# Kernel tuning notes

Measured on AMD Instinct MI355X. Metric: run time of the kernel, lower is better.

## Reference

```python
import jax, jax.numpy as jnp
import numpy as np

GROUPS = 4
BN_EPS = 1e-5


def conv2d(x, w, pad=0):
    return jax.lax.conv_general_dilated(x, w, (1, 1), [(pad, pad), (pad, pad)],
                                        dimension_numbers=('NCHW', 'OIHW', 'NCHW'))


def bn_infer(x, g, b, m, v):
    s = g * jax.lax.rsqrt(v + BN_EPS)
    return x * s[None, :, None, None] + (b - m * s)[None, :, None, None]


def refine_residual(x, w1, w3a, g, b, m, v, w3b):
    # RefineResidual(has_relu=True): 1x1 -> ConvBnRelu(3x3) -> 3x3 conv, residual, relu
    x1 = conv2d(x, w1)
    t = jax.nn.relu(bn_infer(conv2d(x1, w3a, pad=1), g, b, m, v))
    t = conv2d(t, w3b, pad=1)
    return jax.nn.relu(t + x1)


def grid_edges(H, W):
    # 4-connected pixel grid: right + down neighbors
    idx = np.arange(H * W).reshape(H, W)
    eu = np.concatenate([idx[:, :-1].ravel(), idx[:-1, :].ravel()]).astype(np.int32)
    ev = np.concatenate([idx[:, 1:].ravel(), idx[1:, :].ravel()]).astype(np.int32)
    return jnp.asarray(eu), jnp.asarray(ev)


def boruvka_mst(w, eu, ev, N):
    # Boruvka MST over the grid graph; returns bool mask over edges (N-1 True).
    E = w.shape[0]
    nodes = jnp.arange(N, dtype=jnp.int32)
    order = jnp.argsort(w).astype(jnp.int32)                  # edge ids by weight (unique ranks)
    rank = jnp.zeros(E, jnp.int32).at[order].set(jnp.arange(E, dtype=jnp.int32))
    BIG = jnp.int32(E)
    R = int(np.ceil(np.log2(max(N, 2)))) + 2

    def flatten(p):
        return jax.lax.fori_loop(0, R, lambda _, q: q[q], p)

    def body(_, state):
        parent, mst = state
        cu, cv = parent[eu], parent[ev]
        key = jnp.where(cu != cv, rank, BIG)
        cmin = jnp.minimum(jax.ops.segment_min(key, cu, num_segments=N),
                           jax.ops.segment_min(key, cv, num_segments=N))
        valid = cmin < BIG
        e = order[jnp.minimum(cmin, E - 1)]                   # min outgoing edge per component
        mst = mst.at[e].max(valid)
        other = jnp.where(cu[e] == nodes, cv[e], cu[e])
        pnew = jnp.where(valid, other, nodes)
        # break mutual (2-cycle) merges: smaller label becomes root
        pnew = jnp.where((pnew[pnew] == nodes) & (nodes < pnew), nodes, pnew)
        return flatten(pnew), mst

    _, mst = jax.lax.fori_loop(0, R + 2, body, (nodes, jnp.zeros(E, bool)))
    return mst


def root_and_depth(mst, eu, ev, N):
    # BFS-root the tree at node 0 -> parent pointers, then depth by pointer doubling.
    pn = jnp.full(N, -1, jnp.int32).at[0].set(0)

    def bfs(_, pn):
        vis = pn >= 0
        a = mst & vis[eu] & (~vis[ev])
        b = mst & vis[ev] & (~vis[eu])
        pn = pn.at[ev].max(jnp.where(a, eu, jnp.int32(-1)))
        pn = pn.at[eu].max(jnp.where(b, ev, jnp.int32(-1)))
        return pn

    pn = jax.lax.fori_loop(0, N, bfs, pn)
    R = int(np.ceil(np.log2(max(N, 2)))) + 2
    d0 = (jnp.arange(N) != 0).astype(jnp.int32)

    def dbl(_, s):
        d, p = s
        return d + d[p], p[p]

    depth, _ = jax.lax.fori_loop(0, R, dbl, (d0, pn))
    return pn, depth


def tree_filter_group(x, w, pn, depth):
    # Exact O(N) two-pass tree filter: y_i = sum_j prod(path weights i->j) x_j.
    # x: [N, C] (ones channel appended by caller), w: [N] edge weight to parent.
    N = x.shape[0]
    notroot = jnp.arange(N) != 0

    def up(i, agg):                                           # leaves -> root
        lev = N - 1 - i
        sel = (depth == lev) & notroot
        return agg.at[pn].add(jnp.where(sel[:, None], w[:, None] * agg, 0.0))

    agg = jax.lax.fori_loop(0, N - 1, up, x)

    def down(lev, F):                                         # root -> leaves
        cand = agg + w[:, None] * (F[pn] - w[:, None] * agg)
        return jnp.where(((depth == lev) & notroot)[:, None], cand, F)

    return jax.lax.fori_loop(1, N, down, agg)


def tree_filter_2d(feat, emb, pn, depth):
    # Grouped normalized tree filtering (TreeFilter2D): per-group edge affinity
    # exp(-||e_v - e_parent(v)||^2); normalize by filtering an all-ones channel.
    B, C, H, W = feat.shape
    N = H * W
    f = feat.reshape(B, GROUPS, C // GROUPS, N)
    e = emb.reshape(B, GROUPS, -1, N)

    def per_batch(fb, eb, pnb, db):
        w = jnp.exp(-jnp.sum((eb - eb[:, :, pnb]) ** 2, axis=1))   # [G, N]
        x = jnp.concatenate([fb, jnp.ones_like(fb[:, :1])], axis=1)
        x = jnp.swapaxes(x, 1, 2)                                  # [G, N, Cg+1]
        out = jax.vmap(lambda xg, wg: tree_filter_group(xg, wg, pnb, db))(x, w)
        y = out[..., :-1] / out[..., -1:]
        return jnp.swapaxes(y, 1, 2)

    out = jax.vmap(per_batch)(f, e, pn, depth)
    return out.reshape(B, C, H, W)


def _forward(fm, last_fm, lat_w1, lat_w3a, lat_g, lat_b, lat_m, lat_v, lat_w3b,
             ref_w1, ref_w3a, ref_g, ref_b, ref_m, ref_v, ref_w3b, emb_w):
    B, Cb, H, W = fm.shape
    N = H * W
    eu, ev = grid_edges(H, W)
    latent = refine_residual(fm, lat_w1, lat_w3a, lat_g, lat_b, lat_m, lat_v, lat_w3b)
    # MinimumSpanningTree(norm2_distance) on backbone features fm
    f = fm.reshape(B, Cb, N)
    dist = jnp.sum((f[:, :, eu] - f[:, :, ev]) ** 2, axis=1)       # [B, E]
    mst = jax.vmap(lambda d: boruvka_mst(d, eu, ev, N))(dist)
    pn, depth = jax.vmap(lambda m: root_and_depth(m, eu, ev, N))(mst)
    embed = conv2d(last_fm, emb_w)                                 # embed_layer (1x1, no bn/relu)
    fusion = latent + tree_filter_2d(last_fm, embed, pn, depth)
    return refine_residual(fusion, ref_w1, ref_w3a, ref_g, ref_b, ref_m, ref_v, ref_w3b)


def setup_inputs() -> dict:
    key = jax.random.key(0)
    ks = jax.random.split(key, 12)
    B, Cb, Cbiz, Cemb, H, W = 2, 1024, 64, 32, 32, 32
    r = lambda k, s: jax.random.normal(k, s, jnp.float32) * 0.05
    return dict(
        fm=jax.random.normal(ks[0], (B, Cb, H, W), jnp.float32),
        last_fm=jax.random.normal(ks[1], (B, Cbiz, H, W), jnp.float32),
        lat_w1=r(ks[2], (Cbiz, Cb, 1, 1)),
        lat_w3a=r(ks[3], (Cbiz, Cbiz, 3, 3)),
        lat_g=jnp.ones(Cbiz, jnp.float32),
        lat_b=jnp.zeros(Cbiz, jnp.float32),
        lat_m=jnp.zeros(Cbiz, jnp.float32),
        lat_v=jax.random.uniform(ks[4], (Cbiz,), jnp.float32, 0.5, 1.5),
        lat_w3b=r(ks[5], (Cbiz, Cbiz, 3, 3)),
        ref_w1=r(ks[6], (Cbiz, Cbiz, 1, 1)),
        ref_w3a=r(ks[7], (Cbiz, Cbiz, 3, 3)),
        ref_g=jnp.ones(Cbiz, jnp.float32),
        ref_b=jnp.zeros(Cbiz, jnp.float32),
        ref_m=jnp.zeros(Cbiz, jnp.float32),
        ref_v=jax.random.uniform(ks[8], (Cbiz,), jnp.float32, 0.5, 1.5),
        ref_w3b=r(ks[9], (Cbiz, Cbiz, 3, 3)),
        emb_w=r(ks[10], (Cemb, Cbiz, 1, 1)),
    )


def reference(fm, last_fm, lat_w1, lat_w3a, lat_g, lat_b, lat_m, lat_v, lat_w3b,
              ref_w1, ref_w3a, ref_g, ref_b, ref_m, ref_v, ref_w3b, emb_w):
    return _forward(fm, last_fm, lat_w1, lat_w3a, lat_g, lat_b, lat_m, lat_v, lat_w3b,
                    ref_w1, ref_w3a, ref_g, ref_b, ref_m, ref_v, ref_w3b, emb_w)
```

## Files before the change

### kernel.cpp

```cpp
#include <hip/hip_runtime.h>
#include <hip/hip_bf16.h>

#define NN 1024
#define EE 1984

__device__ __forceinline__ void edge_uv(int e, int* u, int* v) {
    if (e < 992) {
        int r = e / 31, c = e - r * 31;
        *u = r * 32 + c; *v = *u + 1;
    } else {
        *u = e - 992; *v = *u + 32;
    }
}

__device__ void conv1x1_tile(const float* __restrict__ in, const float* __restrict__ in2,
                             const float* __restrict__ w,
                             float* __restrict__ out, int CIN, int Cout,
                             int b, int co0, int n0, float* red) {
    int tid = threadIdx.x;
    int px = tid & 63, kc = tid >> 6;
    int kcu = __builtin_amdgcn_readfirstlane(kc);
    int KCH = CIN >> 4;
    size_t ibase = (size_t)b * CIN * NN + n0 + px;
    const float* wr = w + (size_t)co0 * CIN;
    float acc[8] = {0.f,0.f,0.f,0.f,0.f,0.f,0.f,0.f};
    for (int ci = kcu * KCH; ci < kcu * KCH + KCH; ++ci) {
        float xv = in[ibase + (size_t)ci * NN];
        if (in2) xv += in2[ibase + (size_t)ci * NN];
#pragma unroll
        for (int j = 0; j < 8; ++j)
            acc[j] += wr[j * CIN + ci] * xv;
    }
#pragma unroll
    for (int j = 0; j < 8; ++j) red[j * 1024 + tid] = acc[j];
    __syncthreads();
    for (int s = 8; s >= 1; s >>= 1) {
        if (kc < s) {
#pragma unroll
            for (int j = 0; j < 8; ++j)
                red[j * 1024 + kc * 64 + px] += red[j * 1024 + (kc + s) * 64 + px];
        }
        __syncthreads();
    }
    if (kc == 0) {
        size_t ob = ((size_t)b * Cout + co0) * NN + n0 + px;
#pragma unroll
        for (int j = 0; j < 8; ++j) out[ob + (size_t)j * NN] = red[j * 1024 + px];
    }
}

__device__ void dist_tile(const float* __restrict__ fm, float* __restrict__ dist,
                          int b, int eb, float* red) {
    int tid = threadIdx.x;
    int le = tid & 63, kc = tid >> 6;
    int kcu = __builtin_amdgcn_readfirstlane(kc);
    int e = eb * 64 + le;
    int u, v; edge_uv(e, &u, &v);
    const float* fp = fm + (size_t)b * 1024 * NN;
    float s = 0.f;
    for (int c = kcu * 64; c < kcu * 64 + 64; ++c) {
        float d = fp[(size_t)c * NN + u] - fp[(size_t)c * NN + v];
        s += d * d;
    }
    red[tid] = s;
    __syncthreads();
    for (int ss = 8; ss >= 1; ss >>= 1) {
        if (kc < ss) red[kc * 64 + le] += red[(kc + ss) * 64 + le];
        __syncthreads();
    }
    if (kc == 0) dist[b * EE + e] = red[le];
}

__device__ void conv3x3_body(const float* __restrict__ in, const float* __restrict__ w,
                             const float* __restrict__ gg, const float* __restrict__ bb,
                             const float* __restrict__ mm, const float* __restrict__ vv,
                             const float* __restrict__ res, float* __restrict__ out,
                             int mode, int b, int co, int r0, float* pl) {
    int tid = threadIdx.x;
    const float* ip = in + (size_t)b * 64 * NN;
    const float* wp = w + (size_t)co * 64 * 9;
    int r = tid >> 5, c = tid & 31;
    float acc = 0.f;
    for (int h = 0; h < 2; ++h) {
        __syncthreads();
        for (int i4 = tid; i4 < 32 * 80; i4 += 256) {
            int ci = i4 / 80, o = i4 - ci * 80;
            int row = r0 - 1 + (o >> 3), c4 = (o & 7) << 2;
            float4 val = make_float4(0.f, 0.f, 0.f, 0.f);
            if (row >= 0 && row < 32)
                val = *(const float4*)&ip[(size_t)(h * 32 + ci) * NN + row * 32 + c4];
            *(float4*)&pl[ci * 320 + (o >> 3) * 32 + c4] = val;
        }
        __syncthreads();
        for (int ci = 0; ci < 32; ++ci) {
            float wv[9];
#pragma unroll
            for (int q = 0; q < 9; ++q) wv[q] = wp[(h * 32 + ci) * 9 + q];
            float s = 0.f;
#pragma unroll
            for (int dy = 0; dy < 3; ++dy) {
                const float* row = &pl[ci * 320 + (r + dy) * 32];
#pragma unroll
                for (int dx = -1; dx <= 1; ++dx) {
                    int cc = c + dx;
                    float xv = (cc >= 0 && cc < 32) ? row[cc] : 0.f;
                    s += wv[dy * 3 + (dx + 1)] * xv;
                }
            }
            acc += s;
        }
    }
    float val;
    size_t op = ((size_t)b * 64 + co) * NN + r0 * 32 + tid;
    if (mode == 0) {
        float sc = gg[co] * rsqrtf(vv[co] + 1e-5f);
        val = acc * sc + (bb[co] - mm[co] * sc);
    } else {
        val = acc + res[op];
    }
    out[op] = fmaxf(val, 0.f);
}

struct MstS {
    unsigned long long minkey[NN];
    unsigned long long ekey[EE];
    int parent[NN], pnw[NN], pn[NN], dep[NN], scr[NN], elist[NN];
    int mstm[EE];
    int cnt, cnt2;
};

__device__ void mst_body_1024(const float* __restrict__ dist, int b, MstS* S,
                              int* __restrict__ pn_g, int* __restrict__ maxd_g,
                              int* __restrict__ ord_g, int* __restrict__ off_g) {
    int tid = threadIdx.x;
    const float* wb = dist + b * EE;
    S->parent[tid] = tid;
    S->minkey[tid] = ~0ULL;
    for (int e = tid; e < EE; e += 1024) {
        S->mstm[e] = 0;
        S->ekey[e] = ((unsigned long long)__float_as_uint(wb[e]) << 32) | (unsigned)e;
    }
    if (tid == 0) { S->cnt = 0; S->cnt2 = 0; }
    __syncthreads();

    int r = tid >> 5, c = tid & 31;
    for (int round = 0; round < 14; ++round) {
        int pv = S->parent[tid];
        unsigned long long mk = ~0ULL;
        if (c < 31 && S->parent[tid + 1] != pv) {
            unsigned long long k = S->ekey[r * 31 + c];
            if (k < mk) mk = k;
        }
        if (c > 0 && S->parent[tid - 1] != pv) {
            unsigned long long k = S->ekey[r * 31 + c - 1];
            if (k < mk) mk = k;
        }
        if (r < 31 && S->parent[tid + 32] != pv) {
            unsigned long long k = S->ekey[992 + r * 32 + c];
            if (k < mk) mk = k;
        }
        if (r > 0 && S->parent[tid - 32] != pv) {
            unsigned long long k = S->ekey[992 + (r - 1) * 32 + c];
            if (k < mk) mk = k;
        }
        if (mk != ~0ULL) atomicMin(&S->minkey[pv], mk);
        __syncthreads();
        int np;
        unsigned long long sel = S->minkey[tid];
        S->minkey[tid] = ~0ULL;
        if (sel != ~0ULL) {
            int e = (int)(sel & 0xffffffffULL);
            if (atomicExch(&S->mstm[e], 1) == 0) atomicAdd(&S->cnt, 1);
            int eu, ev; edge_uv(e, &eu, &ev);
            int cu = S->parent[eu], cv = S->parent[ev];
            np = (cu == tid) ? cv : cu;
        } else np = tid;
        S->pnw[tid] = np;
        __syncthreads();
        int q = S->pnw[tid];
        int pq = S->pnw[q];
        S->parent[tid] = (pq == tid && tid < q) ? tid : q;
        for (;;) {
            int ch = 0;
            int p = S->parent[tid];
            int pp = S->parent[p];
            if (pp != p) { S->parent[tid] = pp; ch = 1; }
            if (!__syncthreads_or(ch)) break;
        }
        if (S->cnt == NN - 1) break;
    }

    for (int e = tid; e < EE; e += 1024)
        if (S->mstm[e]) { int s = atomicAdd(&S->cnt2, 1); S->elist[s] = e; }
    __syncthreads();
    int ecnt = S->cnt2;

    S->pn[tid] = (tid == 0) ? 0 : -1;
    __syncthreads();
    volatile int* vpn = S->pn;
    int myu = 0, myv = 0; bool have = tid < ecnt;
    if (have) { edge_uv(S->elist[tid], &myu, &myv); }
    for (;;) {
        int ch = 0;
        for (int s = 0; s < 16; ++s) {
            if (have) {
                int pu = vpn[myu], pv = vpn[myv];
                if (pu >= 0 && pv < 0)      { vpn[myv] = myu; ch = 1; }
                else if (pv >= 0 && pu < 0) { vpn[myu] = myv; ch = 1; }
            }
        }
        if (!__syncthreads_or(ch)) break;
    }

    S->dep[tid] = (tid != 0) ? 1 : 0;
    S->pnw[tid] = S->pn[tid];
    __syncthreads();
    int* dA = S->dep; int* dB = S->scr; int* pA = S->pnw; int* pB = S->parent;
    for (int it = 0; it < 12; ++it) {
        int p = pA[tid];
        int j = (p < 0) ? (NN + p) : p;
        dB[tid] = dA[tid] + dA[j];
        pB[tid] = pA[j];
        __syncthreads();
        int* t = dA; dA = dB; dB = t;
        t = pA; pA = pB; pB = t;
    }
    if (tid == 0) S->cnt = 0;
    __syncthreads();
    int d = S->dep[tid];
    if (d >= 1 && d <= NN - 1) atomicMax(&S->cnt, d);
    __syncthreads();
    int maxd = S->cnt;

    S->scr[tid] = 0;
    __syncthreads();
    int bkt = (tid != 0 && d >= 1 && d <= NN - 1) ? d : 0;
    atomicAdd(&S->scr[bkt], 1);
    __syncthreads();
    int cntv = S->scr[tid];
    int lane = tid & 63, wid = tid >> 6;
    int x = cntv;
    for (int d2 = 1; d2 < 64; d2 <<= 1) {
        int y = __shfl_up(x, d2, 64);
        if (lane >= d2) x += y;
    }
    if (lane == 63) S->pnw[wid] = x;
    __syncthreads();
    if (tid < 16) {
        int off = 0;
        for (int i = 0; i < tid; ++i) off += S->pnw[i];
        S->parent[tid] = off;
    }
    __syncthreads();
    int excl = x - cntv + S->parent[wid];
    int* mi = (int*)S->minkey;
    mi[tid] = excl;
    S->scr[tid] = excl;
    __syncthreads();
    int pos = atomicAdd(&S->scr[bkt], 1);
    S->elist[pos] = tid;
    __syncthreads();

    pn_g[b * NN + tid]    = S->pn[tid];
    ord_g[b * NN + tid]   = S->elist[tid];
    off_g[b * 1025 + tid] = mi[tid];
    if (tid == 0) { off_g[b * 1025 + 1024] = NN; maxd_g[b] = maxd; }
}

struct TfSmem { float agg[NN * 3]; float wv[NN]; int jj[NN]; int ords[NN]; int offs[1025]; };
__device__ void treefilter_wave(const float* __restrict__ feat, const float* __restrict__ emb,
                                const int* __restrict__ pn_g, const int* __restrict__ ord_g,
                                const int* __restrict__ off_g, const int* __restrict__ maxd_g,
                                float* __restrict__ tfout, int b, int g, int sub, TfSmem* S) {
    int lane = threadIdx.x;
    const float* eb = emb + ((size_t)b * 32 + g * 8) * NN;
    int c0 = g * 16 + sub * 2;
    const float* fb = feat + ((size_t)b * 64 + c0) * NN;
    for (int k = 0; k < 16; ++k) {
        int v = lane + k * 64;
        int p = pn_g[b * NN + v];
        int j = (p < 0) ? (NN + p) : p;
        S->jj[v] = j;
        float s = 0.f;
#pragma unroll
        for (int q = 0; q < 8; ++q) {
            float d = eb[(size_t)q * NN + v] - eb[(size_t)q * NN + j];
            s += d * d;
        }
        S->wv[v] = expf(-s);
        S->agg[v * 3 + 0] = fb[v];
        S->agg[v * 3 + 1] = fb[NN + v];
        S->agg[v * 3 + 2] = 1.f;
        S->ords[v] = ord_g[b * NN + v];
        S->offs[v] = off_g[b * 1025 + v];
    }
    if (lane == 0) S->offs[1024] = NN;
    int maxdep = maxd_g[b];
    for (int lev = maxdep; lev >= 1; --lev) {
        int s0 = S->offs[lev], s1 = S->offs[lev + 1];
        for (int i = s0 + lane; i < s1; i += 64) {
            int v = S->ords[i]; int j = S->jj[v]; float w = S->wv[v];
            atomicAdd(&S->agg[j * 3 + 0], w * S->agg[v * 3 + 0]);
            atomicAdd(&S->agg[j * 3 + 1], w * S->agg[v * 3 + 1]);
            atomicAdd(&S->agg[j * 3 + 2], w * S->agg[v * 3 + 2]);
        }
    }
    for (int lev = 1; lev <= maxdep; ++lev) {
        int s0 = S->offs[lev], s1 = S->offs[lev + 1];
        for (int i = s0 + lane; i < s1; i += 64) {
            int v = S->ords[i]; int j = S->jj[v]; float w = S->wv[v];
#pragma unroll
            for (int c = 0; c < 3; ++c) {
                float a = S->agg[v * 3 + c];
                S->agg[v * 3 + c] = a + w * (S->agg[j * 3 + c] - w * a);
            }
        }
    }
    float* ob = tfout + ((size_t)b * 64 + c0) * NN;
    for (int k = 0; k < 16; ++k) {
        int v = lane + k * 64;
        float inv = 1.f / S->agg[v * 3 + 2];
        ob[v]      = S->agg[v * 3 + 0] * inv;
        ob[NN + v] = S->agg[v * 3 + 1] * inv;
    }
}

__global__ __launch_bounds__(1024) void k0_dist(
    const float* __restrict__ fm, float* __restrict__ dist) {
    __shared__ float red[1024];
    int i = blockIdx.x;
    dist_tile(fm, dist, i / 31, i % 31, red);
}

union K1S { float red[8192]; MstS m; };
__global__ __launch_bounds__(1024) void k1_fused(
    const float* __restrict__ fm, const float* __restrict__ last_fm,
    const float* __restrict__ lat_w1, const float* __restrict__ emb_w,
    float* __restrict__ lat_x1, float* __restrict__ embed,
    const float* __restrict__ dist, int* __restrict__ pn_g,
    int* __restrict__ maxd_g, int* __restrict__ ord_g, int* __restrict__ off_g) {
    __shared__ __align__(16) K1S s;
    int bx = blockIdx.x;
    if (bx < 2) {
        mst_body_1024(dist, bx, &s.m, pn_g, maxd_g, ord_g, off_g);
    } else if (bx < 258) {
        int i = bx - 2, b = i >> 7, r = i & 127;
        conv1x1_tile(fm, nullptr, lat_w1, lat_x1, 1024, 64,
                     b, (r >> 4) * 8, (r & 15) * 64, s.red);
    } else {
        int i = bx - 258, b = i >> 6, r = i & 63;
        conv1x1_tile(last_fm, nullptr, emb_w, embed, 64, 32,
                     b, (r >> 4) * 8, (r & 15) * 64, s.red);
    }
}

union K2S { float pl[32 * 320]; TfSmem t; };
__global__ __launch_bounds__(256) void k2_fused(
    const float* __restrict__ lat_x1, const float* __restrict__ lat_w3a,
    const float* __restrict__ lat_g, const float* __restrict__ lat_b,
    const float* __restrict__ lat_m, const float* __restrict__ lat_v,
    float* __restrict__ lat_t1,
    const float* __restrict__ last_fm, const float* __restrict__ embed,
    const int* __restrict__ pn_g, const int* __restrict__ ord_g,
    const int* __restrict__ off_g, const int* __restrict__ maxd_g,
    float* __restrict__ tfout) {
    __shared__ __align__(16) K2S s;
    int bx = blockIdx.x;
    if (bx < 64) {
        if (threadIdx.x >= 64) return;
        treefilter_wave(last_fm, embed, pn_g, ord_g, off_g, maxd_g, tfout,
                        bx >> 5, (bx >> 3) & 3, bx & 7, &s.t);
    } else {
        int i = bx - 64, b = i >> 8, co = (i >> 2) & 63, r0 = (i & 3) * 8;
        conv3x3_body(lat_x1, lat_w3a, lat_g, lat_b, lat_m, lat_v,
                     nullptr, lat_t1, 0, b, co, r0, s.pl);
    }
}

__global__ __launch_bounds__(256) void conv3x3_kernel(
    const float* __restrict__ in, const float* __restrict__ w,
    const float* __restrict__ gg, const float* __restrict__ bb,
    const float* __restrict__ mm, const float* __restrict__ vv,
    const float* __restrict__ res, float* __restrict__ out, int mode) {
    __shared__ __align__(16) float pl[32 * 320];
    conv3x3_body(in, w, gg, bb, mm, vv, res, out, mode,
                 blockIdx.z, blockIdx.y, blockIdx.x * 8, pl);
}

__global__ __launch_bounds__(1024) void conv1x1_add_kernel(
    const float* __restrict__ in, const float* __restrict__ in2,
    const float* __restrict__ w, float* __restrict__ out, int CIN, int Cout) {
    __shared__ float red[8192];
    conv1x1_tile(in, in2, w, out, CIN, Cout, blockIdx.z, blockIdx.y * 8,
                 blockIdx.x * 64, red);
}

extern "C" void kernel_launch(void* const* d_in, const int* in_sizes, int n_in,
                              void* d_out, int out_size, void* d_ws, size_t ws_size,
                              hipStream_t stream) {
    const float* fm      = (const float*)d_in[0];
    const float* last_fm = (const float*)d_in[1];
    const float* lat_w1  = (const float*)d_in[2];
    const float* lat_w3a = (const float*)d_in[3];
    const float* lat_g   = (const float*)d_in[4];
    const float* lat_b   = (const float*)d_in[5];
    const float* lat_m   = (const float*)d_in[6];
    const float* lat_v   = (const float*)d_in[7];
    const float* lat_w3b = (const float*)d_in[8];
    const float* ref_w1  = (const float*)d_in[9];
    const float* ref_w3a = (const float*)d_in[10];
    const float* ref_g   = (const float*)d_in[11];
    const float* ref_b   = (const float*)d_in[12];
    const float* ref_m   = (const float*)d_in[13];
    const float* ref_v   = (const float*)d_in[14];
    const float* ref_w3b = (const float*)d_in[15];
    const float* emb_w   = (const float*)d_in[16];
    float* out = (float*)d_out;

    float* ws      = (float*)d_ws;
    float* lat_x1  = ws;
    float* lat_t1  = lat_x1 + 131072;
    float* latent  = lat_t1 + 131072;
    float* dist    = latent + 131072;
    float* embed   = dist + 4096;
    float* tfout   = embed + 65536;
    float* ref_x1  = tfout + 131072;
    float* ref_t1  = ref_x1 + 131072;
    int*   pn      = (int*)(ref_t1 + 131072);
    int*   ordg    = pn + 2048;
    int*   offg    = ordg + 2048;
    int*   maxd    = offg + 2080;

    k0_dist<<<62, 1024, 0, stream>>>(fm, dist);
    k1_fused<<<386, 1024, 0, stream>>>(fm, last_fm, lat_w1, emb_w,
                                       lat_x1, embed, dist, pn, maxd, ordg, offg);
    k2_fused<<<576, 256, 0, stream>>>(lat_x1, lat_w3a, lat_g, lat_b, lat_m, lat_v,
                                      lat_t1, last_fm, embed, pn, ordg, offg,
                                      maxd, tfout);
    conv3x3_kernel<<<dim3(4, 64, 2), 256, 0, stream>>>(
        lat_t1, lat_w3b, nullptr, nullptr, nullptr, nullptr, lat_x1, latent, 1);
    conv1x1_add_kernel<<<dim3(16, 8, 2), 1024, 0, stream>>>(
        latent, tfout, ref_w1, ref_x1, 64, 64);
    conv3x3_kernel<<<dim3(4, 64, 2), 256, 0, stream>>>(
        ref_x1, ref_w3a, ref_g, ref_b, ref_m, ref_v, nullptr, ref_t1, 0);
    conv3x3_kernel<<<dim3(4, 64, 2), 256, 0, stream>>>(
        ref_t1, ref_w3b, nullptr, nullptr, nullptr, nullptr, ref_x1, out, 1);
}
```

Measured before the change: 241.0 us.

## Reschedule kernels: merge dist with 1x1 convs, overlap MST with lateral 3x3 conv

The distance computation moves into the same launch as the two 1x1 convolutions. The MST is rewritten to run in a 256-thread block, each thread handling four nodes, so it can share a launch with the first lateral 3x3 conv. The second lateral 3x3 conv moves into the tree-filter launch, which drops one kernel launch overall. Pointer jumping now takes two hops per iteration, and the depth-doubling loop can exit early once every parent pointer has reached the root. The sequential MST now runs with fewer threads per block, which risks a longer critical path if it dominates the launch it shares.

```diff
diff --git a/kernel.cpp b/kernel.cpp
--- a/kernel.cpp
+++ b/kernel.cpp
@@ -129,141 +129,211 @@
     int cnt, cnt2;
 };
 
-__device__ void mst_body_1024(const float* __restrict__ dist, int b, MstS* S,
-                              int* __restrict__ pn_g, int* __restrict__ maxd_g,
-                              int* __restrict__ ord_g, int* __restrict__ off_g) {
+__device__ void mst_body_256(const float* __restrict__ dist, int b, MstS* S,
+                             int* __restrict__ pn_g, int* __restrict__ maxd_g,
+                             int* __restrict__ ord_g, int* __restrict__ off_g) {
     int tid = threadIdx.x;
     const float* wb = dist + b * EE;
-    S->parent[tid] = tid;
-    S->minkey[tid] = ~0ULL;
-    for (int e = tid; e < EE; e += 1024) {
+#pragma unroll
+    for (int k = 0; k < 4; ++k) {
+        int v = tid + k * 256;
+        S->parent[v] = v;
+        S->minkey[v] = ~0ULL;
+    }
+    for (int e = tid; e < EE; e += 256) {
         S->mstm[e] = 0;
         S->ekey[e] = ((unsigned long long)__float_as_uint(wb[e]) << 32) | (unsigned)e;
     }
     if (tid == 0) { S->cnt = 0; S->cnt2 = 0; }
     __syncthreads();
 
-    int r = tid >> 5, c = tid & 31;
     for (int round = 0; round < 14; ++round) {
-        int pv = S->parent[tid];
-        unsigned long long mk = ~0ULL;
-        if (c < 31 && S->parent[tid + 1] != pv) {
-            unsigned long long k = S->ekey[r * 31 + c];
-            if (k < mk) mk = k;
-        }
-        if (c > 0 && S->parent[tid - 1] != pv) {
-            unsigned long long k = S->ekey[r * 31 + c - 1];
-            if (k < mk) mk = k;
-        }
-        if (r < 31 && S->parent[tid + 32] != pv) {
-            unsigned long long k = S->ekey[992 + r * 32 + c];
-            if (k < mk) mk = k;
-        }
-        if (r > 0 && S->parent[tid - 32] != pv) {
-            unsigned long long k = S->ekey[992 + (r - 1) * 32 + c];
-            if (k < mk) mk = k;
-        }
-        if (mk != ~0ULL) atomicMin(&S->minkey[pv], mk);
-        __syncthreads();
-        int np;
-        unsigned long long sel = S->minkey[tid];
-        S->minkey[tid] = ~0ULL;
-        if (sel != ~0ULL) {
-            int e = (int)(sel & 0xffffffffULL);
-            if (atomicExch(&S->mstm[e], 1) == 0) atomicAdd(&S->cnt, 1);
-            int eu, ev; edge_uv(e, &eu, &ev);
-            int cu = S->parent[eu], cv = S->parent[ev];
-            np = (cu == tid) ? cv : cu;
-        } else np = tid;
-        S->pnw[tid] = np;
-        __syncthreads();
-        int q = S->pnw[tid];
-        int pq = S->pnw[q];
-        S->parent[tid] = (pq == tid && tid < q) ? tid : q;
+#pragma unroll
+        for (int k = 0; k < 4; ++k) {
+            int v = tid + k * 256;
+            int r = v >> 5, c = v & 31;
+            int pv = S->parent[v];
+            unsigned long long mk = ~0ULL;
+            if (c < 31 && S->parent[v + 1] != pv) {
+                unsigned long long kk = S->ekey[r * 31 + c]; if (kk < mk) mk = kk;
+            }
+            if (c > 0 && S->parent[v - 1] != pv) {
+                unsigned long long kk = S->ekey[r * 31 + c - 1]; if (kk < mk) mk = kk;
+            }
+            if (r < 31 && S->parent[v + 32] != pv) {
+                unsigned long long kk = S->ekey[992 + r * 32 + c]; if (kk < mk) mk = kk;
+            }
+            if (r > 0 && S->parent[v - 32] != pv) {
+                unsigned long long kk = S->ekey[992 + (r - 1) * 32 + c]; if (kk < mk) mk = kk;
+            }
+            if (mk != ~0ULL) atomicMin(&S->minkey[pv], mk);
+        }
+        __syncthreads();
+#pragma unroll
+        for (int k = 0; k < 4; ++k) {
+            int v = tid + k * 256;
+            int np;
+            unsigned long long sel = S->minkey[v];
+            S->minkey[v] = ~0ULL;
+            if (sel != ~0ULL) {
+                int e = (int)(sel & 0xffffffffULL);
+                if (atomicExch(&S->mstm[e], 1) == 0) atomicAdd(&S->cnt, 1);
+                int eu, ev; edge_uv(e, &eu, &ev);
+                int cu = S->parent[eu], cv = S->parent[ev];
+                np = (cu == v) ? cv : cu;
+            } else np = v;
+            S->pnw[v] = np;
+        }
+        __syncthreads();
+#pragma unroll
+        for (int k = 0; k < 4; ++k) {
+            int v = tid + k * 256;
+            int q = S->pnw[v];
+            int pq = S->pnw[q];
+            S->parent[v] = (pq == v && v < q) ? v : q;
+        }
+        __syncthreads();
         for (;;) {
             int ch = 0;
-            int p = S->parent[tid];
-            int pp = S->parent[p];
-            if (pp != p) { S->parent[tid] = pp; ch = 1; }
+#pragma unroll
+            for (int k = 0; k < 4; ++k) {
+                int v = tid + k * 256;
+                int p = S->parent[v];
+                p = S->parent[p];
+                p = S->parent[p];
+                S->parent[v] = p;
+                if (S->parent[p] != p) ch = 1;
+            }
             if (!__syncthreads_or(ch)) break;
         }
         if (S->cnt == NN - 1) break;
     }
 
-    for (int e = tid; e < EE; e += 1024)
+    for (int e = tid; e < EE; e += 256)
         if (S->mstm[e]) { int s = atomicAdd(&S->cnt2, 1); S->elist[s] = e; }
     __syncthreads();
     int ecnt = S->cnt2;
 
-    S->pn[tid] = (tid == 0) ? 0 : -1;
+#pragma unroll
+    for (int k = 0; k < 4; ++k) { int v = tid + k * 256; S->pn[v] = (v == 0) ? 0 : -1; }
     __syncthreads();
     volatile int* vpn = S->pn;
-    int myu = 0, myv = 0; bool have = tid < ecnt;
-    if (have) { edge_uv(S->elist[tid], &myu, &myv); }
+    int eu_[4], ev_[4];
+    bool have[4];
+#pragma unroll
+    for (int k = 0; k < 4; ++k) {
+        int idx = tid + k * 256;
+        have[k] = idx < ecnt;
+        eu_[k] = 0; ev_[k] = 0;
+        if (have[k]) edge_uv(S->elist[idx], &eu_[k], &ev_[k]);
+    }
     for (;;) {
         int ch = 0;
         for (int s = 0; s < 16; ++s) {
-            if (have) {
-                int pu = vpn[myu], pv = vpn[myv];
-                if (pu >= 0 && pv < 0)      { vpn[myv] = myu; ch = 1; }
-                else if (pv >= 0 && pu < 0) { vpn[myu] = myv; ch = 1; }
+#pragma unroll
+            for (int k = 0; k < 4; ++k) {
+                if (have[k]) {
+                    int pu = vpn[eu_[k]], pv = vpn[ev_[k]];
+                    if (pu >= 0 && pv < 0)      { vpn[ev_[k]] = eu_[k]; ch = 1; }
+                    else if (pv >= 0 && pu < 0) { vpn[eu_[k]] = ev_[k]; ch = 1; }
+                }
             }
         }
         if (!__syncthreads_or(ch)) break;
     }
-
-    S->dep[tid] = (tid != 0) ? 1 : 0;
-    S->pnw[tid] = S->pn[tid];
-    __syncthreads();
-    int* dA = S->dep; int* dB = S->scr; int* pA = S->pnw; int* pB = S->parent;
+    int incomplete = __syncthreads_or((S->pn[tid] < 0) | (S->pn[tid + 256] < 0) |
+                                      (S->pn[tid + 512] < 0) | (S->pn[tid + 768] < 0));
+
+#pragma unroll
+    for (int k = 0; k < 4; ++k) {
+        int v = tid + k * 256;
+        S->dep[v] = (v != 0) ? 1 : 0;
+        S->pnw[v] = S->pn[v];
+    }
+    __syncthreads();
+    int* dA = S->dep;                  int* dB = (int*)S->ekey;
+    int* pA = S->pnw;                  int* pB = ((int*)S->ekey) + NN;
     for (int it = 0; it < 12; ++it) {
-        int p = pA[tid];
-        int j = (p < 0) ? (NN + p) : p;
-        dB[tid] = dA[tid] + dA[j];
-        pB[tid] = pA[j];
-        __syncthreads();
+        int allz = 1;
+#pragma unroll
+        for (int k = 0; k < 4; ++k) {
+            int v = tid + k * 256;
+            int p = pA[v];
+            int j = (p < 0) ? (NN + p) : p;
+            dB[v] = dA[v] + dA[j];
+            int nx = pA[j];
+            pB[v] = nx;
+            if (nx != 0) allz = 0;
+        }
+        int fin = (!incomplete) && (!__syncthreads_or(!allz));
         int* t = dA; dA = dB; dB = t;
         t = pA; pA = pB; pB = t;
+        if (fin) break;
     }
     if (tid == 0) S->cnt = 0;
     __syncthreads();
-    int d = S->dep[tid];
-    if (d >= 1 && d <= NN - 1) atomicMax(&S->cnt, d);
+    int dloc[4], lm = 0;
+#pragma unroll
+    for (int k = 0; k < 4; ++k) {
+        dloc[k] = dA[tid + k * 256];
+        if (dloc[k] >= 1 && dloc[k] <= NN - 1 && dloc[k] > lm) lm = dloc[k];
+    }
+    atomicMax(&S->cnt, lm);
+#pragma unroll
+    for (int k = 0; k < 4; ++k) S->scr[tid + k * 256] = 0;
     __syncthreads();
     int maxd = S->cnt;
-
-    S->scr[tid] = 0;
-    __syncthreads();
-    int bkt = (tid != 0 && d >= 1 && d <= NN - 1) ? d : 0;
-    atomicAdd(&S->scr[bkt], 1);
-    __syncthreads();
-    int cntv = S->scr[tid];
+    int bkt[4];
+#pragma unroll
+    for (int k = 0; k < 4; ++k) {
+        int v = tid + k * 256;
+        bkt[k] = (v != 0 && dloc[k] >= 1 && dloc[k] <= NN - 1) ? dloc[k] : 0;
+        atomicAdd(&S->scr[bkt[k]], 1);
+    }
+    __syncthreads();
+    int base = tid * 4;
+    int c0 = S->scr[base], c1 = S->scr[base + 1], c2 = S->scr[base + 2], c3 = S->scr[base + 3];
+    int run = c0 + c1 + c2 + c3;
     int lane = tid & 63, wid = tid >> 6;
-    int x = cntv;
+    int x = run;
     for (int d2 = 1; d2 < 64; d2 <<= 1) {
         int y = __shfl_up(x, d2, 64);
         if (lane >= d2) x += y;
     }
     if (lane == 63) S->pnw[wid] = x;
     __syncthreads();
-    if (tid < 16) {
+    if (tid < 4) {
         int off = 0;
         for (int i = 0; i < tid; ++i) off += S->pnw[i];
         S->parent[tid] = off;
     }
     __syncthreads();
-    int excl = x - cntv + S->parent[wid];
+    int excl = x - run + S->parent[wid];
     int* mi = (int*)S->minkey;
-    mi[tid] = excl;
-    S->scr[tid] = excl;
-    __syncthreads();
-    int pos = atomicAdd(&S->scr[bkt], 1);
-    S->elist[pos] = tid;
-    __syncthreads();
-
-    pn_g[b * NN + tid]    = S->pn[tid];
-    ord_g[b * NN + tid]   = S->elist[tid];
-    off_g[b * 1025 + tid] = mi[tid];
+    mi[base]     = excl;
+    mi[base + 1] = excl + c0;
+    mi[base + 2] = excl + c0 + c1;
+    mi[base + 3] = excl + c0 + c1 + c2;
+    S->scr[base]     = mi[base];
+    S->scr[base + 1] = mi[base + 1];
+    S->scr[base + 2] = mi[base + 2];
+    S->scr[base + 3] = mi[base + 3];
+    __syncthreads();
+#pragma unroll
+    for (int k = 0; k < 4; ++k) {
+        int v = tid + k * 256;
+        int pos = atomicAdd(&S->scr[bkt[k]], 1);
+        S->elist[pos] = v;
+    }
+    __syncthreads();
+
+#pragma unroll
+    for (int k = 0; k < 4; ++k) {
+        int v = tid + k * 256;
+        pn_g[b * NN + v]    = S->pn[v];
+        ord_g[b * NN + v]   = S->elist[v];
+        off_g[b * 1025 + v] = mi[v];
+    }
     if (tid == 0) { off_g[b * 1025 + 1024] = NN; maxd_g[b] = maxd; }
 }
 
@@ -325,45 +395,52 @@
     }
 }
 
-__global__ __launch_bounds__(1024) void k0_dist(
-    const float* __restrict__ fm, float* __restrict__ dist) {
-    __shared__ float red[1024];
-    int i = blockIdx.x;
-    dist_tile(fm, dist, i / 31, i % 31, red);
-}
-
-union K1S { float red[8192]; MstS m; };
-__global__ __launch_bounds__(1024) void k1_fused(
+__global__ __launch_bounds__(1024) void k0_fused(
     const float* __restrict__ fm, const float* __restrict__ last_fm,
     const float* __restrict__ lat_w1, const float* __restrict__ emb_w,
-    float* __restrict__ lat_x1, float* __restrict__ embed,
+    float* __restrict__ lat_x1, float* __restrict__ embed, float* __restrict__ dist) {
+    __shared__ __align__(16) float red[8192];
+    int bx = blockIdx.x;
+    if (bx < 62) {
+        dist_tile(fm, dist, bx / 31, bx % 31, red);
+    } else if (bx < 318) {
+        int i = bx - 62, b = i >> 7, r = i & 127;
+        conv1x1_tile(fm, nullptr, lat_w1, lat_x1, 1024, 64,
+                     b, (r >> 4) * 8, (r & 15) * 64, red);
+    } else {
+        int i = bx - 318, b = i >> 6, r = i & 63;
+        conv1x1_tile(last_fm, nullptr, emb_w, embed, 64, 32,
+                     b, (r >> 4) * 8, (r & 15) * 64, red);
+    }
+}
+
+union K1S { float pl[32 * 320]; MstS m; };
+__global__ __launch_bounds__(256) void k1_fused(
     const float* __restrict__ dist, int* __restrict__ pn_g,
-    int* __restrict__ maxd_g, int* __restrict__ ord_g, int* __restrict__ off_g) {
+    int* __restrict__ maxd_g, int* __restrict__ ord_g, int* __restrict__ off_g,
+    const float* __restrict__ lat_x1, const float* __restrict__ lat_w3a,
+    const float* __restrict__ lat_g, const float* __restrict__ lat_b,
+    const float* __restrict__ lat_m, const float* __restrict__ lat_v,
+    float* __restrict__ lat_t1) {
     __shared__ __align__(16) K1S s;
     int bx = blockIdx.x;
     if (bx < 2) {
-        mst_body_1024(dist, bx, &s.m, pn_g, maxd_g, ord_g, off_g);
-    } else if (bx < 258) {
-        int i = bx - 2, b = i >> 7, r = i & 127;
-        conv1x1_tile(fm, nullptr, lat_w1, lat_x1, 1024, 64,
-                     b, (r >> 4) * 8, (r & 15) * 64, s.red);
+        mst_body_256(dist, bx, &s.m, pn_g, maxd_g, ord_g, off_g);
     } else {
-        int i = bx - 258, b = i >> 6, r = i & 63;
-        conv1x1_tile(last_fm, nullptr, emb_w, embed, 64, 32,
-                     b, (r >> 4) * 8, (r & 15) * 64, s.red);
+        int i = bx - 2, b = i >> 8, co = (i >> 2) & 63, r0 = (i & 3) * 8;
+        conv3x3_body(lat_x1, lat_w3a, lat_g, lat_b, lat_m, lat_v,
+                     nullptr, lat_t1, 0, b, co, r0, s.pl);
     }
 }
 
 union K2S { float pl[32 * 320]; TfSmem t; };
 __global__ __launch_bounds__(256) void k2_fused(
-    const float* __restrict__ lat_x1, const float* __restrict__ lat_w3a,
-    const float* __restrict__ lat_g, const float* __restrict__ lat_b,
-    const float* __restrict__ lat_m, const float* __restrict__ lat_v,
-    float* __restrict__ lat_t1,
     const float* __restrict__ last_fm, const float* __restrict__ embed,
     const int* __restrict__ pn_g, const int* __restrict__ ord_g,
     const int* __restrict__ off_g, const int* __restrict__ maxd_g,
-    float* __restrict__ tfout) {
+    float* __restrict__ tfout,
+    const float* __restrict__ lat_t1, const float* __restrict__ lat_w3b,
+    const float* __restrict__ lat_x1, float* __restrict__ latent) {
     __shared__ __align__(16) K2S s;
     int bx = blockIdx.x;
     if (bx < 64) {
@@ -372,8 +449,8 @@
                         bx >> 5, (bx >> 3) & 3, bx & 7, &s.t);
     } else {
         int i = bx - 64, b = i >> 8, co = (i >> 2) & 63, r0 = (i & 3) * 8;
-        conv3x3_body(lat_x1, lat_w3a, lat_g, lat_b, lat_m, lat_v,
-                     nullptr, lat_t1, 0, b, co, r0, s.pl);
+        conv3x3_body(lat_t1, lat_w3b, nullptr, nullptr, nullptr, nullptr,
+                     lat_x1, latent, 1, b, co, r0, s.pl);
     }
 }
 
@@ -431,14 +508,13 @@
     int*   offg    = ordg + 2048;
     int*   maxd    = offg + 2080;
 
-    k0_dist<<<62, 1024, 0, stream>>>(fm, dist);
-    k1_fused<<<386, 1024, 0, stream>>>(fm, last_fm, lat_w1, emb_w,
-                                       lat_x1, embed, dist, pn, maxd, ordg, offg);
-    k2_fused<<<576, 256, 0, stream>>>(lat_x1, lat_w3a, lat_g, lat_b, lat_m, lat_v,
-                                      lat_t1, last_fm, embed, pn, ordg, offg,
-                                      maxd, tfout);
-    conv3x3_kernel<<<dim3(4, 64, 2), 256, 0, stream>>>(
-        lat_t1, lat_w3b, nullptr, nullptr, nullptr, nullptr, lat_x1, latent, 1);
+    k0_fused<<<446, 1024, 0, stream>>>(fm, last_fm, lat_w1, emb_w,
+                                       lat_x1, embed, dist);
+    k1_fused<<<514, 256, 0, stream>>>(dist, pn, maxd, ordg, offg,
+                                      lat_x1, lat_w3a, lat_g, lat_b, lat_m, lat_v,
+                                      lat_t1);
+    k2_fused<<<576, 256, 0, stream>>>(last_fm, embed, pn, ordg, offg, maxd,
+                                      tfout, lat_t1, lat_w3b, lat_x1, latent);
     conv1x1_add_kernel<<<dim3(16, 8, 2), 1024, 0, stream>>>(
         latent, tfout, ref_w1, ref_x1, 64, 64);
     conv3x3_kernel<<<dim3(4, 64, 2), 256, 0, stream>>>(
```

New measurement: 259.4 us. 1.08x slower.

## Cut barriers in Boruvka MST rounds and exit pointer jumping early

Applied to the files above, without the earlier changes.

Each Boruvka round now works out the 2-cycle-breaking parent directly from the neighbour component's selected edge, which removes one barrier. Parent arrays are double-buffered and the pointer-jumping loop takes several hops per barrier. The depth-doubling loop stops early once every pointer reaches the root, with a guard for an incomplete tree, and the BFS inner loop runs more steps per barrier. The aim is fewer __syncthreads in a serial, latency-bound single-block phase, at the cost of more complex logic that also reuses ekey as scratch space.

```diff
diff --git a/kernel.cpp b/kernel.cpp
--- a/kernel.cpp
+++ b/kernel.cpp
@@ -144,50 +144,60 @@
     __syncthreads();
 
     int r = tid >> 5, c = tid & 31;
+    int* P = S->parent;
+    int* Q = S->pnw;
     for (int round = 0; round < 14; ++round) {
-        int pv = S->parent[tid];
+        int pv = P[tid];
         unsigned long long mk = ~0ULL;
-        if (c < 31 && S->parent[tid + 1] != pv) {
-            unsigned long long k = S->ekey[r * 31 + c];
-            if (k < mk) mk = k;
-        }
-        if (c > 0 && S->parent[tid - 1] != pv) {
-            unsigned long long k = S->ekey[r * 31 + c - 1];
-            if (k < mk) mk = k;
-        }
-        if (r < 31 && S->parent[tid + 32] != pv) {
-            unsigned long long k = S->ekey[992 + r * 32 + c];
-            if (k < mk) mk = k;
-        }
-        if (r > 0 && S->parent[tid - 32] != pv) {
-            unsigned long long k = S->ekey[992 + (r - 1) * 32 + c];
-            if (k < mk) mk = k;
+        if (c < 31 && P[tid + 1] != pv) {
+            unsigned long long k = S->ekey[r * 31 + c]; if (k < mk) mk = k;
+        }
+        if (c > 0 && P[tid - 1] != pv) {
+            unsigned long long k = S->ekey[r * 31 + c - 1]; if (k < mk) mk = k;
+        }
+        if (r < 31 && P[tid + 32] != pv) {
+            unsigned long long k = S->ekey[992 + r * 32 + c]; if (k < mk) mk = k;
+        }
+        if (r > 0 && P[tid - 32] != pv) {
+            unsigned long long k = S->ekey[992 + (r - 1) * 32 + c]; if (k < mk) mk = k;
         }
         if (mk != ~0ULL) atomicMin(&S->minkey[pv], mk);
         __syncthreads();
+
+        unsigned long long sel = S->minkey[tid];
         int np;
-        unsigned long long sel = S->minkey[tid];
-        S->minkey[tid] = ~0ULL;
         if (sel != ~0ULL) {
             int e = (int)(sel & 0xffffffffULL);
             if (atomicExch(&S->mstm[e], 1) == 0) atomicAdd(&S->cnt, 1);
             int eu, ev; edge_uv(e, &eu, &ev);
-            int cu = S->parent[eu], cv = S->parent[ev];
+            int cu = P[eu], cv = P[ev];
             np = (cu == tid) ? cv : cu;
         } else np = tid;
-        S->pnw[tid] = np;
-        __syncthreads();
-        int q = S->pnw[tid];
-        int pq = S->pnw[q];
-        S->parent[tid] = (pq == tid && tid < q) ? tid : q;
+        int q = np, pq;
+        if (q == tid) pq = tid;
+        else {
+            unsigned long long selq = S->minkey[q];
+            if (selq != ~0ULL) {
+                int e2 = (int)(selq & 0xffffffffULL);
+                int eu2, ev2; edge_uv(e2, &eu2, &ev2);
+                int cu2 = P[eu2], cv2 = P[ev2];
+                pq = (cu2 == q) ? cv2 : cu2;
+            } else pq = q;
+        }
+        Q[tid] = (pq == tid && tid < q) ? tid : q;
+        __syncthreads();
+
+        bool first = true;
         for (;;) {
-            int ch = 0;
-            int p = S->parent[tid];
-            int pp = S->parent[p];
-            if (pp != p) { S->parent[tid] = pp; ch = 1; }
+            if (first) { S->minkey[tid] = ~0ULL; first = false; }
+            int p = Q[tid];
+            p = Q[p]; p = Q[p]; p = Q[p];
+            Q[tid] = p;
+            int ch = (Q[p] != p);
             if (!__syncthreads_or(ch)) break;
         }
         if (S->cnt == NN - 1) break;
+        int* t = P; P = Q; Q = t;
     }
 
     for (int e = tid; e < EE; e += 1024)
@@ -202,7 +212,7 @@
     if (have) { edge_uv(S->elist[tid], &myu, &myv); }
     for (;;) {
         int ch = 0;
-        for (int s = 0; s < 16; ++s) {
+        for (int s = 0; s < 24; ++s) {
             if (have) {
                 int pu = vpn[myu], pv = vpn[myv];
                 if (pu >= 0 && pv < 0)      { vpn[myv] = myu; ch = 1; }
@@ -211,23 +221,27 @@
         }
         if (!__syncthreads_or(ch)) break;
     }
+    int incomplete = __syncthreads_or(S->pn[tid] < 0);
 
     S->dep[tid] = (tid != 0) ? 1 : 0;
     S->pnw[tid] = S->pn[tid];
     __syncthreads();
-    int* dA = S->dep; int* dB = S->scr; int* pA = S->pnw; int* pB = S->parent;
+    int* dA = S->dep;  int* dB = (int*)S->ekey;
+    int* pA = S->pnw;  int* pB = ((int*)S->ekey) + NN;
     for (int it = 0; it < 12; ++it) {
         int p = pA[tid];
         int j = (p < 0) ? (NN + p) : p;
         dB[tid] = dA[tid] + dA[j];
-        pB[tid] = pA[j];
-        __syncthreads();
+        int nx = pA[j];
+        pB[tid] = nx;
+        int anynz = __syncthreads_or(nx != 0);
         int* t = dA; dA = dB; dB = t;
         t = pA; pA = pB; pB = t;
+        if (!incomplete && !anynz) break;
     }
     if (tid == 0) S->cnt = 0;
     __syncthreads();
-    int d = S->dep[tid];
+    int d = dA[tid];
     if (d >= 1 && d <= NN - 1) atomicMax(&S->cnt, d);
     __syncthreads();
     int maxd = S->cnt;
```

Result: no change. 244.3 us (+1.4%).
